# Performance work log

Measured on AMD Instinct MI355X. Metric: run time of the kernel, lower is better.

The kernel has to match this reference:

```python
import jax, jax.numpy as jnp
import numpy as np

COMMITMENT_COST = 0.25


def setup_inputs() -> dict:
    key = jax.random.key(0)
    k1, k2 = jax.random.split(key)
    inputs = jax.random.normal(k1, (32, 512, 32, 32), dtype=jnp.float32)
    embeddings = jax.random.normal(k2, (4096, 512), dtype=jnp.float32)
    return {"inputs": inputs, "embeddings": embeddings}


def reference(inputs, embeddings):
    # NCHW -> NHWC, flatten to (N, D)
    x = jnp.transpose(inputs, (0, 2, 3, 1))  # [B,H,W,D]
    D = embeddings.shape[1]
    z = x.reshape(-1, D)  # [N,D]

    # Squared L2 distances: ||z||^2 - 2 z E^T + ||E||^2
    d1 = jnp.sum(z * z, axis=1, keepdims=True)            # [N,1]
    d2 = 2.0 * jnp.matmul(z, embeddings.T)                # [N,K]
    d3 = jnp.sum(embeddings * embeddings, axis=1)[None]   # [1,K]
    distances = d1 - d2 + d3                              # [N,K]

    k = jnp.argmin(distances, axis=1)                     # [N]
    q = embeddings[k]                                     # [N,D] gather

    # latent loss: codebook loss + commitment loss
    e_loss = jnp.mean((jax.lax.stop_gradient(z) - q) ** 2)
    q_loss = COMMITMENT_COST * jnp.mean((z - jax.lax.stop_gradient(q)) ** 2)
    loss = e_loss + q_loss

    qx = q.reshape(x.shape)                               # [B,H,W,D]
    output = jnp.transpose(qx, (0, 3, 1, 2))              # NCHW
    return output, loss
```

## Files before the change

kernel.cpp:

```cpp
#include <hip/hip_runtime.h>

#define N_PTS 32768
#define DIM   512
#define KCODES 4096
#define HW    1024
#define MARGIN 0.125f
#define MAXFLAG 2048

typedef _Float16 half8 __attribute__((ext_vector_type(8)));
typedef float f32x4 __attribute__((ext_vector_type(4)));
typedef unsigned long long u64;

#define E16_OFF   0
#define BIAS_OFF  4194304
#define TOP2_OFF  4210688
#define ZC_OFF    5259264


__device__ __forceinline__ unsigned mono(float f) {
    unsigned u = __float_as_uint(f);
    return (u & 0x80000000u) ? ~u : (u | 0x80000000u);
}
__device__ __forceinline__ float unmono(unsigned m) {
    unsigned u = (m & 0x80000000u) ? (m & 0x7FFFFFFFu) : ~m;
    return __uint_as_float(u);
}

#define ASYNC16(src, dst) __builtin_amdgcn_global_load_lds( \
    (const __attribute__((address_space(1))) void*)(src), \
    (__attribute__((address_space(3))) void*)(dst), 16, 0, 0)

__global__ void prep_e_kernel(const float* __restrict__ E, _Float16* __restrict__ E16,
                              float* __restrict__ bias) {
    int k = blockIdx.x;
    int l = threadIdx.x;
    const float4* row = (const float4*)(E + (size_t)k * DIM);
    float4 a = row[l * 2];
    float4 b = row[l * 2 + 1];
    half8 h;
    h[0] = (_Float16)a.x; h[1] = (_Float16)a.y; h[2] = (_Float16)a.z; h[3] = (_Float16)a.w;
    h[4] = (_Float16)b.x; h[5] = (_Float16)b.y; h[6] = (_Float16)b.z; h[7] = (_Float16)b.w;
    *(half8*)(E16 + (size_t)k * DIM + l * 8) = h;
    float s = a.x * a.x + a.y * a.y + a.z * a.z + a.w * a.w +
              b.x * b.x + b.y * b.y + b.z * b.z + b.w * b.w;
#pragma unroll
    for (int off = 32; off > 0; off >>= 1) s += __shfl_down(s, off, 64);
    if (l == 0) bias[k] = 0.5f * s;
}

__global__ __launch_bounds__(256, 2) void score16_kernel(
    const float* __restrict__ in, const _Float16* __restrict__ E16,
    const float* __restrict__ bias, u64* __restrict__ top2)
{
    __shared__ alignas(16) _Float16 stage[2048 * 8];

    const int t    = threadIdx.x;
    const int lane = t & 63;
    const int w    = t >> 6;
    const int lm   = lane & 15;
    const int lq   = lane >> 4;
    const int ks   = blockIdx.x;
    const int pt0  = blockIdx.y * 128;

    half8 zf[2][16];
#pragma unroll
    for (int pt = 0; pt < 2; pt++) {
        const int n = pt0 + 32 * w + 16 * pt + lm;
        const float* zb = in + (size_t)(n >> 10) * (DIM * HW) + (n & 1023);
#pragma unroll
        for (int kc = 0; kc < 16; kc++) {
            const int d0 = kc * 32 + lq * 8;
            half8 h;
#pragma unroll
            for (int j = 0; j < 8; j++) h[j] = (_Float16)zb[(size_t)(d0 + j) << 10];
            zf[pt][kc] = h;
        }
    }

    const u64 PKNEG = ((u64)0x007FFFFFu) << 32;
    u64 b1[2], b2[2];
    float thr2[2];
#pragma unroll
    for (int p = 0; p < 2; p++) { b1[p] = PKNEG; b2[p] = PKNEG; thr2[p] = -INFINITY; }

    for (int f = 0; f < 64; f++) {
        const int code0 = ks * 2048 + f * 32;
#pragma unroll
        for (int i = 0; i < 8; i++) {
            const int kc = 4 * w + (i >> 1);
            const int ct = i & 1;
            const _Float16* src = E16 + (size_t)(code0 + ct * 16 + lm) * DIM + kc * 32 + lq * 8;
            ASYNC16(src, stage + ((size_t)(w * 512 + i * 64) << 3));
        }
        __syncthreads();
        f32x4 acc[2][2];
#pragma unroll
        for (int ct = 0; ct < 2; ct++) {
            const float4 bv = *(const float4*)&bias[code0 + ct * 16 + lq * 4];
            f32x4 bi; bi[0] = -bv.x; bi[1] = -bv.y; bi[2] = -bv.z; bi[3] = -bv.w;
            acc[ct][0] = bi; acc[ct][1] = bi;
        }
#pragma unroll
        for (int kc = 0; kc < 16; kc++) {
            half8 a0 = *(const half8*)&stage[(size_t)(kc * 128 + lane) << 3];
            half8 a1 = *(const half8*)&stage[(size_t)(kc * 128 + 64 + lane) << 3];
            acc[0][0] = __builtin_amdgcn_mfma_f32_16x16x32_f16(a0, zf[0][kc], acc[0][0], 0, 0, 0);
            acc[0][1] = __builtin_amdgcn_mfma_f32_16x16x32_f16(a0, zf[1][kc], acc[0][1], 0, 0, 0);
            acc[1][0] = __builtin_amdgcn_mfma_f32_16x16x32_f16(a1, zf[0][kc], acc[1][0], 0, 0, 0);
            acc[1][1] = __builtin_amdgcn_mfma_f32_16x16x32_f16(a1, zf[1][kc], acc[1][1], 0, 0, 0);
        }
        __syncthreads();
#pragma unroll
        for (int pt = 0; pt < 2; pt++) {
#pragma unroll
            for (int ct = 0; ct < 2; ct++) {
                f32x4 a = acc[ct][pt];
                bool hit = (a[0] > thr2[pt]) | (a[1] > thr2[pt]) |
                           (a[2] > thr2[pt]) | (a[3] > thr2[pt]);
                if (__any(hit)) {
#pragma unroll
                    for (int r = 0; r < 4; r++) {
                        float v = a[r];
                        if (v > thr2[pt]) {
                            int code = code0 + ct * 16 + lq * 4 + r;
                            u64 pk = ((u64)mono(v) << 32) | (unsigned)(0xFFFu ^ (unsigned)code);
                            if (pk > b1[pt]) { b2[pt] = b1[pt]; b1[pt] = pk; }
                            else if (pk > b2[pt]) { b2[pt] = pk; }
                            thr2[pt] = unmono((unsigned)(b2[pt] >> 32));
                        }
                    }
                }
            }
        }
    }
#pragma unroll
    for (int pt = 0; pt < 2; pt++) {
#pragma unroll
        for (int m = 16; m <= 32; m <<= 1) {
            u64 o1 = __shfl_xor(b1[pt], m, 64);
            u64 o2 = __shfl_xor(b2[pt], m, 64);
            u64 m1 = b1[pt] > o1 ? b1[pt] : o1;
            u64 lo = b1[pt] > o1 ? o1 : b1[pt];
            u64 mm = b2[pt] > o2 ? b2[pt] : o2;
            b2[pt] = lo > mm ? lo : mm;
            b1[pt] = m1;
        }
    }
    if (lq == 0) {
#pragma unroll
        for (int pt = 0; pt < 2; pt++) {
            const size_t p = (size_t)(pt0 + 32 * w + 16 * pt + lm);
            top2[p * 4 + ks * 2]     = b1[pt];
            top2[p * 4 + ks * 2 + 1] = b2[pt];
        }
    }
}

__global__ void merge_kernel(const u64* __restrict__ top2, int* __restrict__ k_final,
                             int* __restrict__ list, int* __restrict__ count) {
    int pt = blockIdx.x * 256 + threadIdx.x;
    const u64* p = top2 + (size_t)pt * 4;
    u64 B1 = 0, B2 = 0;
#pragma unroll
    for (int ks = 0; ks < 2; ks++) {
        u64 p1 = p[ks * 2], p2 = p[ks * 2 + 1];
        u64 m1 = B1 > p1 ? B1 : p1;
        u64 lo = B1 > p1 ? p1 : B1;
        u64 mm = B2 > p2 ? B2 : p2;
        B2 = lo > mm ? lo : mm;
        B1 = m1;
    }
    k_final[pt] = 0xFFF ^ (int)(B1 & 0xFFFull);
    float s1 = unmono((unsigned)(B1 >> 32));
    float s2 = unmono((unsigned)(B2 >> 32));
    if (s1 - s2 < MARGIN) {
        int idx = atomicAdd(count, 1);
        if (idx < MAXFLAG) list[idx] = pt;
    }
}

__global__ void compact_kernel(const float* __restrict__ in, const int* __restrict__ list,
                               const int* __restrict__ count, float* __restrict__ zc) {
    int cnt = *count; if (cnt > MAXFLAG) cnt = MAXFLAG;
    const int w = threadIdx.x >> 6;
    const int l = threadIdx.x & 63;
    const int i = blockIdx.x * 4 + w;
    if (i >= cnt) return;
    const int pt = list[i];
    const float* zb = in + (size_t)(pt >> 10) * (DIM * HW) + (pt & 1023);
    float v[8];
#pragma unroll
    for (int j = 0; j < 8; j++) v[j] = zb[(size_t)(l * 8 + j) << 10];
    float4* dst = (float4*)(zc + (size_t)i * DIM + l * 8);
    dst[0] = make_float4(v[0], v[1], v[2], v[3]);
    dst[1] = make_float4(v[4], v[5], v[6], v[7]);
}

__global__ __launch_bounds__(256) void rescore_kernel(
    const float* __restrict__ zc, const float* __restrict__ E,
    const float* __restrict__ bias, const int* __restrict__ count,
    u64* __restrict__ rb)
{
    __shared__ float As[16][128];
    __shared__ float Bs[16][132];

    int cnt = *count; if (cnt > MAXFLAG) cnt = MAXFLAG;
    const int t  = threadIdx.x;
    const int k0 = blockIdx.x * 128;
    const int r0 = blockIdx.y * 128;
    if (r0 >= cnt) return;

    float acc[8][8];
#pragma unroll
    for (int i = 0; i < 8; i++)
#pragma unroll
        for (int j = 0; j < 8; j++) acc[i][j] = 0.f;

    const int ra = (t >> 4) << 2;
    const int cb = (t & 15) << 2;

    for (int d0 = 0; d0 < DIM; d0 += 16) {
        {
            int j   = t >> 2;
            int dd4 = (t & 3) << 2;
            int rA = r0 + j;        if (rA >= cnt) rA = cnt - 1;
            int rB = r0 + j + 64;   if (rB >= cnt) rB = cnt - 1;
            float4 v0 = *(const float4*)&zc[(size_t)rA * DIM + d0 + dd4];
            float4 v1 = *(const float4*)&zc[(size_t)rB * DIM + d0 + dd4];
            As[dd4 + 0][j] = v0.x; As[dd4 + 1][j] = v0.y;
            As[dd4 + 2][j] = v0.z; As[dd4 + 3][j] = v0.w;
            As[dd4 + 0][j + 64] = v1.x; As[dd4 + 1][j + 64] = v1.y;
            As[dd4 + 2][j + 64] = v1.z; As[dd4 + 3][j + 64] = v1.w;
        }
        {
            int j   = t >> 2;
            int dd4 = (t & 3) << 2;
            const float* p = E + (size_t)(k0 + j) * DIM + d0 + dd4;
            float4 v0 = *(const float4*)p;
            float4 v1 = *(const float4*)(p + (size_t)64 * DIM);
            Bs[dd4 + 0][j] = v0.x; Bs[dd4 + 1][j] = v0.y;
            Bs[dd4 + 2][j] = v0.z; Bs[dd4 + 3][j] = v0.w;
            Bs[dd4 + 0][j + 64] = v1.x; Bs[dd4 + 1][j + 64] = v1.y;
            Bs[dd4 + 2][j + 64] = v1.z; Bs[dd4 + 3][j + 64] = v1.w;
        }
        __syncthreads();
#pragma unroll
        for (int dd = 0; dd < 16; dd++) {
            float4 a0 = *(const float4*)&As[dd][ra];
            float4 a1 = *(const float4*)&As[dd][ra + 64];
            float4 b0 = *(const float4*)&Bs[dd][cb];
            float4 b1v = *(const float4*)&Bs[dd][cb + 64];
            float av[8] = {a0.x, a0.y, a0.z, a0.w, a1.x, a1.y, a1.z, a1.w};
            float bv[8] = {b0.x, b0.y, b0.z, b0.w, b1v.x, b1v.y, b1v.z, b1v.w};
#pragma unroll
            for (int i = 0; i < 8; i++)
#pragma unroll
                for (int j = 0; j < 8; j++)
                    acc[i][j] = fmaf(av[i], bv[j], acc[i][j]);
        }
        __syncthreads();
    }

    float bcol[8];
#pragma unroll
    for (int j = 0; j < 8; j++) {
        int k = k0 + ((j < 4) ? (cb + j) : (64 + cb + j - 4));
        bcol[j] = bias[k];
    }
    u64 pk[8];
#pragma unroll
    for (int i = 0; i < 8; i++) {
        u64 bestp = 0ull;
#pragma unroll
        for (int j = 0; j < 8; j++) {
            int k = k0 + ((j < 4) ? (cb + j) : (64 + cb + j - 4));
            float s = acc[i][j] - bcol[j];
            u64 p = ((u64)mono(s) << 32) | (u64)(~(unsigned)k);
            if (p > bestp) bestp = p;
        }
        pk[i] = bestp;
    }
#pragma unroll
    for (int i = 0; i < 8; i++) {
#pragma unroll
        for (int off = 8; off > 0; off >>= 1) {
            u64 o = __shfl_down(pk[i], off, 16);
            if (o > pk[i]) pk[i] = o;
        }
    }
    if ((t & 15) == 0) {
#pragma unroll
        for (int i = 0; i < 8; i++) {
            int row = r0 + ((i < 4) ? (ra + i) : (64 + ra + i - 4));
            int slot = row < cnt ? row : cnt - 1;
            atomicMax(&rb[slot], pk[i]);
        }
    }
}

__global__ void apply_kernel(const int* __restrict__ list, const int* __restrict__ count,
                             const u64* __restrict__ rb, int* __restrict__ k_final) {
    int i = blockIdx.x * 256 + threadIdx.x;
    int cnt = *count; if (cnt > MAXFLAG) cnt = MAXFLAG;
    if (i < cnt) k_final[list[i]] = (int)(~(unsigned)(rb[i] & 0xffffffffull));
}

__global__ void gather_kernel(const float* __restrict__ in, const float* __restrict__ E,
                              const int* __restrict__ k_final,
                              float* __restrict__ out, float* __restrict__ sumsq)
{
    const int t  = threadIdx.x;
    const int tx = t & 63;
    const int ty = t >> 6;
    const int n  = blockIdx.x * 64 + tx;
    const int k  = k_final[n];
    const float* erow = E + (size_t)k * DIM;
    const size_t base = (size_t)(n >> 10) * (DIM * HW) + (n & 1023);
    float local = 0.f;
    for (int d = ty; d < DIM; d += 4) {
        float q = erow[d];
        size_t idx = base + ((size_t)d << 10);
        float z = in[idx];
        out[idx] = q;
        float df = z - q;
        local = fmaf(df, df, local);
    }
#pragma unroll
    for (int off = 32; off > 0; off >>= 1) local += __shfl_down(local, off, 64);
    __shared__ float red[4];
    if (tx == 0) red[ty] = local;
    __syncthreads();
    if (t == 0) atomicAdd(sumsq, red[0] + red[1] + red[2] + red[3]);
}

__global__ void finalize_kernel(const float* __restrict__ sumsq, float* __restrict__ out_loss) {
    *out_loss = 1.25f * (*sumsq) * (1.0f / 16777216.0f);
}

extern "C" void kernel_launch(void* const* d_in, const int* in_sizes, int n_in,
                              void* d_out, int out_size, void* d_ws, size_t ws_size,
                              hipStream_t stream) {
    const float* in = (const float*)d_in[0];
    const float* E  = (const float*)d_in[1];
    float* out = (float*)d_out;
    char* ob = (char*)d_out;

    _Float16* E16 = (_Float16*)(ob + E16_OFF);
    float* bias   = (float*)(ob + BIAS_OFF);
    u64* top2     = (u64*)(ob + TOP2_OFF);
    float* zc     = (float*)(ob + ZC_OFF);

    int* k_final = (int*)d_ws;
    int* list    = (int*)((char*)d_ws + 131072);
    u64* rb      = (u64*)((char*)d_ws + 139264);
    int* count   = (int*)((char*)d_ws + 155648);
    float* sumsq = (float*)((char*)d_ws + 155652);

    hipMemsetAsync(d_ws, 0, 155656, stream);

    prep_e_kernel<<<KCODES, 64, 0, stream>>>(E, E16, bias);

    score16_kernel<<<dim3(2, 256), 256, 0, stream>>>(in, E16, bias, top2);

    merge_kernel<<<128, 256, 0, stream>>>(top2, k_final, list, count);

    compact_kernel<<<512, 256, 0, stream>>>(in, list, count, zc);
    rescore_kernel<<<dim3(32, 16), 256, 0, stream>>>(zc, E, bias, count, rb);
    apply_kernel<<<8, 256, 0, stream>>>(list, count, rb, k_final);

    gather_kernel<<<N_PTS / 64, 256, 0, stream>>>(in, E, k_final, out, sumsq);
    finalize_kernel<<<1, 1, 0, stream>>>(sumsq, out + 16777216);
}
```

Before: 523.4 us.

## Double-buffer codebook staging in score kernel and fuse merge with compaction

The score kernel now uses two LDS stage buffers, prefetching the next 32-code tile asynchronously while computing on the current one, and drops one barrier per iteration. The merge and compact kernels are fused, so each flagged point's thread copies its 512-element column directly into the compacted buffer. The workspace is rearranged so that only the rb, count and sumsq region is memset rather than the whole k_final region. Risks: LDS use doubles, which may limit occupancy at 2 blocks per CU. The fused copy is serial per thread, with strided, uncoalesced loads and writes. The prefetch wraps on the last iteration and issues a redundant load.

After: 504.4 us. -3.6%, faster.

```diff
diff --git a/kernel.cpp b/kernel.cpp
--- a/kernel.cpp
+++ b/kernel.cpp
@@ -52,7 +52,7 @@
     const float* __restrict__ in, const _Float16* __restrict__ E16,
     const float* __restrict__ bias, u64* __restrict__ top2)
 {
-    __shared__ alignas(16) _Float16 stage[2048 * 8];
+    __shared__ alignas(16) _Float16 stage[2][2048 * 8];
 
     const int t    = threadIdx.x;
     const int lane = t & 63;
@@ -83,16 +83,31 @@
 #pragma unroll
     for (int p = 0; p < 2; p++) { b1[p] = PKNEG; b2[p] = PKNEG; thr2[p] = -INFINITY; }
 
-    for (int f = 0; f < 64; f++) {
-        const int code0 = ks * 2048 + f * 32;
+    {
+        const int code0 = ks * 2048;
 #pragma unroll
         for (int i = 0; i < 8; i++) {
             const int kc = 4 * w + (i >> 1);
             const int ct = i & 1;
-            const _Float16* src = E16 + (size_t)(code0 + ct * 16 + lm) * DIM + kc * 32 + lq * 8;
-            ASYNC16(src, stage + ((size_t)(w * 512 + i * 64) << 3));
-        }
+            ASYNC16(E16 + (size_t)(code0 + ct * 16 + lm) * DIM + kc * 32 + lq * 8,
+                    &stage[0][(size_t)(w * 512 + i * 64) << 3]);
+        }
+    }
+
+    for (int f = 0; f < 64; f++) {
+        const int code0 = ks * 2048 + f * 32;
+        const int buf = f & 1;
         __syncthreads();
+        {
+            const int cn = ks * 2048 + ((f + 1) & 63) * 32;
+#pragma unroll
+            for (int i = 0; i < 8; i++) {
+                const int kc = 4 * w + (i >> 1);
+                const int ct = i & 1;
+                ASYNC16(E16 + (size_t)(cn + ct * 16 + lm) * DIM + kc * 32 + lq * 8,
+                        &stage[buf ^ 1][(size_t)(w * 512 + i * 64) << 3]);
+            }
+        }
         f32x4 acc[2][2];
 #pragma unroll
         for (int ct = 0; ct < 2; ct++) {
@@ -102,14 +117,13 @@
         }
 #pragma unroll
         for (int kc = 0; kc < 16; kc++) {
-            half8 a0 = *(const half8*)&stage[(size_t)(kc * 128 + lane) << 3];
-            half8 a1 = *(const half8*)&stage[(size_t)(kc * 128 + 64 + lane) << 3];
+            half8 a0 = *(const half8*)&stage[buf][(size_t)(kc * 128 + lane) << 3];
+            half8 a1 = *(const half8*)&stage[buf][(size_t)(kc * 128 + 64 + lane) << 3];
             acc[0][0] = __builtin_amdgcn_mfma_f32_16x16x32_f16(a0, zf[0][kc], acc[0][0], 0, 0, 0);
             acc[0][1] = __builtin_amdgcn_mfma_f32_16x16x32_f16(a0, zf[1][kc], acc[0][1], 0, 0, 0);
             acc[1][0] = __builtin_amdgcn_mfma_f32_16x16x32_f16(a1, zf[0][kc], acc[1][0], 0, 0, 0);
             acc[1][1] = __builtin_amdgcn_mfma_f32_16x16x32_f16(a1, zf[1][kc], acc[1][1], 0, 0, 0);
         }
-        __syncthreads();
 #pragma unroll
         for (int pt = 0; pt < 2; pt++) {
 #pragma unroll
@@ -156,8 +170,9 @@
     }
 }
 
-__global__ void merge_kernel(const u64* __restrict__ top2, int* __restrict__ k_final,
-                             int* __restrict__ list, int* __restrict__ count) {
+__global__ void merge_compact_kernel(const u64* __restrict__ top2, const float* __restrict__ in,
+                                     int* __restrict__ k_final, int* __restrict__ list,
+                                     int* __restrict__ count, float* __restrict__ zc) {
     int pt = blockIdx.x * 256 + threadIdx.x;
     const u64* p = top2 + (size_t)pt * 4;
     u64 B1 = 0, B2 = 0;
@@ -175,25 +190,14 @@
     float s2 = unmono((unsigned)(B2 >> 32));
     if (s1 - s2 < MARGIN) {
         int idx = atomicAdd(count, 1);
-        if (idx < MAXFLAG) list[idx] = pt;
-    }
-}
-
-__global__ void compact_kernel(const float* __restrict__ in, const int* __restrict__ list,
-                               const int* __restrict__ count, float* __restrict__ zc) {
-    int cnt = *count; if (cnt > MAXFLAG) cnt = MAXFLAG;
-    const int w = threadIdx.x >> 6;
-    const int l = threadIdx.x & 63;
-    const int i = blockIdx.x * 4 + w;
-    if (i >= cnt) return;
-    const int pt = list[i];
-    const float* zb = in + (size_t)(pt >> 10) * (DIM * HW) + (pt & 1023);
-    float v[8];
-#pragma unroll
-    for (int j = 0; j < 8; j++) v[j] = zb[(size_t)(l * 8 + j) << 10];
-    float4* dst = (float4*)(zc + (size_t)i * DIM + l * 8);
-    dst[0] = make_float4(v[0], v[1], v[2], v[3]);
-    dst[1] = make_float4(v[4], v[5], v[6], v[7]);
+        if (idx < MAXFLAG) {
+            list[idx] = pt;
+            const float* zb = in + (size_t)(pt >> 10) * (DIM * HW) + (pt & 1023);
+            float* dst = zc + (size_t)idx * DIM;
+#pragma unroll 8
+            for (int d = 0; d < DIM; d++) dst[d] = zb[(size_t)d << 10];
+        }
+    }
 }
 
 __global__ __launch_bounds__(256) void rescore_kernel(
@@ -350,21 +354,20 @@
     u64* top2     = (u64*)(ob + TOP2_OFF);
     float* zc     = (float*)(ob + ZC_OFF);
 
-    int* k_final = (int*)d_ws;
-    int* list    = (int*)((char*)d_ws + 131072);
-    u64* rb      = (u64*)((char*)d_ws + 139264);
-    int* count   = (int*)((char*)d_ws + 155648);
-    float* sumsq = (float*)((char*)d_ws + 155652);
-
-    hipMemsetAsync(d_ws, 0, 155656, stream);
+    u64* rb      = (u64*)d_ws;
+    int* count   = (int*)((char*)d_ws + 16384);
+    float* sumsq = (float*)((char*)d_ws + 16388);
+    int* list    = (int*)((char*)d_ws + 16392);
+    int* k_final = (int*)((char*)d_ws + 24584);
+
+    hipMemsetAsync(d_ws, 0, 16392, stream);
 
     prep_e_kernel<<<KCODES, 64, 0, stream>>>(E, E16, bias);
 
     score16_kernel<<<dim3(2, 256), 256, 0, stream>>>(in, E16, bias, top2);
 
-    merge_kernel<<<128, 256, 0, stream>>>(top2, k_final, list, count);
-
-    compact_kernel<<<512, 256, 0, stream>>>(in, list, count, zc);
+    merge_compact_kernel<<<128, 256, 0, stream>>>(top2, in, k_final, list, count, zc);
+
     rescore_kernel<<<dim3(32, 16), 256, 0, stream>>>(zc, E, bias, count, rb);
     apply_kernel<<<8, 256, 0, stream>>>(list, count, rb, k_final);
 
```
